# Kernel optimization log

Measured on AMD Instinct MI355X. Metric: run time of the kernel, lower is better.

## Reference

```python
import jax, jax.numpy as jnp
import numpy as np

B, S, E, H, NQ, FF = 4, 1024, 256, 32, 8, 1024
DK = E // H  # 8, equals n_wires of the quantum attention layer
EPS = 1e-5


def layernorm(x, g, b):
    mu = jnp.mean(x, axis=-1, keepdims=True)
    var = jnp.mean(jnp.square(x - mu), axis=-1, keepdims=True)
    return (x - mu) * jax.lax.rsqrt(var + EPS) * g + b


def setup_inputs() -> dict:
    key = jax.random.key(0)
    ks = jax.random.split(key, 20)
    s = lambda n: 1.0 / np.sqrt(n)
    return {
        "x": jax.random.normal(ks[0], (B, S, E), dtype=jnp.float32),
        # quantum attention trainable RX angles (one per wire)
        "theta_attn": jax.random.uniform(ks[1], (DK,), minval=-np.pi, maxval=np.pi),
        # nn.MultiheadAttention packed in-proj and out-proj
        "w_in": jax.random.normal(ks[2], (3 * E, E)) * s(E),
        "b_in": jnp.zeros((3 * E,), jnp.float32),
        "w_out": jax.random.normal(ks[3], (E, E)) * s(E),
        "b_out": jnp.zeros((E,), jnp.float32),
        # combine linear
        "w_comb": jax.random.normal(ks[4], (E, E)) * s(E),
        "b_comb": jnp.zeros((E,), jnp.float32),
        # layernorms
        "g1": jnp.ones((E,), jnp.float32), "be1": jnp.zeros((E,), jnp.float32),
        "g2": jnp.ones((E,), jnp.float32), "be2": jnp.zeros((E,), jnp.float32),
        # FFN: input_proj, quantum RY angles, linear1, linear2
        "w_ip": jax.random.normal(ks[5], (NQ, E)) * s(E),
        "b_ip": jnp.zeros((NQ,), jnp.float32),
        "theta_ffn": jax.random.uniform(ks[6], (NQ,), minval=-np.pi, maxval=np.pi),
        "w1": jax.random.normal(ks[7], (FF, NQ)) * s(NQ),
        "b1": jnp.zeros((FF,), jnp.float32),
        "w2": jax.random.normal(ks[8], (E, FF)) * s(FF),
        "b2": jnp.zeros((E,), jnp.float32),
    }


def reference(x, theta_attn, w_in, b_in, w_out, b_out, w_comb, b_comb,
              g1, be1, g2, be2, w_ip, b_ip, theta_ffn, w1, b1, w2, b2):
    batch, seq, embed = x.shape
    # ---- QuantumAttention ----
    # per-head RX(x_i) encoding followed by trainable RX(theta_i): <Z_i> = cos(x_i + theta_i)
    xh = x.reshape(batch, seq, H, DK)            # [B,S,H,dk]
    q_out = jnp.cos(xh + theta_attn).reshape(batch, seq, embed)
    # standard multi-head self-attention on q_out (q=k=v)
    qkv = q_out @ w_in.T + b_in                  # [B,S,3E]
    q, k, v = jnp.split(qkv, 3, axis=-1)
    def heads(t):
        return t.reshape(batch, seq, H, DK).transpose(0, 2, 1, 3)  # [B,H,S,dk]
    q, k, v = heads(q), heads(k), heads(v)
    scores = jnp.einsum('bhqd,bhkd->bhqk', q, k) / np.sqrt(DK)
    attn = jax.nn.softmax(scores, axis=-1)
    ctx = jnp.einsum('bhqk,bhkd->bhqd', attn, v)
    ctx = ctx.transpose(0, 2, 1, 3).reshape(batch, seq, embed)
    attn_out = (ctx @ w_out.T + b_out) @ w_comb.T + b_comb
    # ---- residual + norm1 ----
    h = layernorm(x + attn_out, g1, be1)
    # ---- QuantumFeedForward ----
    proj = h @ w_ip.T + b_ip                     # [B,S,NQ]
    # RX(x) encoding then trainable RY(phi): <Z> = cos(phi) * cos(x)
    qf = jnp.cos(theta_ffn) * jnp.cos(proj)
    ffn_out = jax.nn.relu(qf @ w1.T + b1) @ w2.T + b2
    # ---- residual + norm2 ----
    return layernorm(h + ffn_out, g2, be2)
```

## Files before the change

kernel.cpp:

```cpp
#include <hip/hip_runtime.h>
#include <hip/hip_bf16.h>

#define B_  4
#define S_  1024
#define E_  256
#define H_  32
#define DK_ 8
#define NQ_ 8
#define FF_ 1024
#define M_  (B_*S_)
#define QS  0.5100880289202462f

typedef __attribute__((ext_vector_type(8))) short bf16x8;
typedef __attribute__((ext_vector_type(4))) short short4v;
typedef __attribute__((ext_vector_type(4))) float f32x4;

__device__ inline short f2bf(float f) {
    union { float f; unsigned u; } v; v.f = f;
    unsigned r = (v.u + 0x7fff + ((v.u >> 16) & 1)) >> 16;
    return (short)r;
}

__device__ inline unsigned pk2(float a, float b) {
    __hip_bfloat162 h = __float22bfloat162_rn(make_float2(a, b));
    union { __hip_bfloat162 h; unsigned u; } c; c.h = h;
    return c.u;
}

__global__ __launch_bounds__(256) void prep_kernel(
        const float* __restrict__ x, const float* __restrict__ theta_attn,
        const float* __restrict__ w_in, const float* __restrict__ b_in,
        const float* __restrict__ w_out, const float* __restrict__ w_comb,
        const float* __restrict__ b_out, const float* __restrict__ b_comb,
        const float* __restrict__ w2,
        ushort* __restrict__ qout_bf, ushort* __restrict__ w_in_bf,
        float* __restrict__ b_in_s, ushort* __restrict__ w2_bf,
        ushort* __restrict__ w_comb_bf, ushort* __restrict__ w_outT_bf,
        float* __restrict__ zeros256, float* __restrict__ beff) {
    int blk = blockIdx.x, tid = threadIdx.x;
    __shared__ float red[4];
    if (blk < 512) {
        int i = blk * 256 + tid;
        float4 a = ((const float4*)x)[i * 2];
        float4 b = ((const float4*)x)[i * 2 + 1];
        bf16x8 o;
        o[0] = f2bf(__cosf(a.x + theta_attn[0]));
        o[1] = f2bf(__cosf(a.y + theta_attn[1]));
        o[2] = f2bf(__cosf(a.z + theta_attn[2]));
        o[3] = f2bf(__cosf(a.w + theta_attn[3]));
        o[4] = f2bf(__cosf(b.x + theta_attn[4]));
        o[5] = f2bf(__cosf(b.y + theta_attn[5]));
        o[6] = f2bf(__cosf(b.z + theta_attn[6]));
        o[7] = f2bf(__cosf(b.w + theta_attn[7]));
        *(bf16x8*)(qout_bf + (size_t)i * 8) = o;
    } else if (blk < 704) {
        int i = (blk - 512) * 256 + tid;
        float sc = (i < 16384) ? QS : 1.f;
        float4 v = ((const float4*)w_in)[i];
        short4v o = {f2bf(v.x * sc), f2bf(v.y * sc), f2bf(v.z * sc), f2bf(v.w * sc)};
        ((short4v*)w_in_bf)[i] = o;
    } else if (blk < 960) {
        int i = (blk - 704) * 256 + tid;
        float4 v = ((const float4*)w2)[i];
        short4v o = {f2bf(v.x), f2bf(v.y), f2bf(v.z), f2bf(v.w)};
        ((short4v*)w2_bf)[i] = o;
    } else if (blk < 1024) {
        int i = (blk - 960) * 256 + tid;
        float4 v = ((const float4*)w_comb)[i];
        short4v o = {f2bf(v.x), f2bf(v.y), f2bf(v.z), f2bf(v.w)};
        ((short4v*)w_comb_bf)[i] = o;
    } else if (blk < 1088) {
        int idx = (blk - 1024) * 256 + tid;
        int e = idx * 4, j = e >> 8, k0 = e & 255;
        short4v o;
#pragma unroll
        for (int i2 = 0; i2 < 4; ++i2) o[i2] = f2bf(w_out[(size_t)(k0 + i2) * 256 + j]);
        *(short4v*)(w_outT_bf + j * 256 + k0) = o;
    } else if (blk < 1089) {
        for (int r = 0; r < 3; ++r) {
            int i = r * 256 + tid;
            b_in_s[i] = b_in[i] * ((i < 256) ? QS : 1.f);
        }
        zeros256[tid] = 0.f;
    } else {
        int i = blk - 1089;
        float p = w_comb[(size_t)i * 256 + tid] * b_out[tid];
#pragma unroll
        for (int o = 32; o > 0; o >>= 1) p += __shfl_xor(p, o);
        if ((tid & 63) == 0) red[tid >> 6] = p;
        __syncthreads();
        if (tid == 0) beff[i] = red[0] + red[1] + red[2] + red[3] + b_comb[i];
    }
}

template<int OUT_BF16>
__global__ __launch_bounds__(256) void gemm_mfma_kernel(const ushort* __restrict__ A,
                                                        const ushort* __restrict__ W,
                                                        const float* __restrict__ bias,
                                                        void* __restrict__ Cv,
                                                        int Ndim, int Kdim) {
    __shared__ ushort As[128 * 64];
    __shared__ ushort Bs[64 * 64];
    int bm = blockIdx.y * 128, bn = blockIdx.x * 64;
    int tid = threadIdx.x;
    int w = tid >> 6, l = tid & 63, lq = l & 15, hi = l >> 4;
    int wm = w & 1, wn = w >> 1;
    f32x4 acc[4][2] = {};
    int srow = tid >> 3;
    int skb = (tid & 7) * 16;

    for (int k0 = 0; k0 < Kdim; k0 += 64) {
        __syncthreads();
#pragma unroll
        for (int it = 0; it < 4; ++it) {
            int row = it * 32 + srow;
            bf16x8 v = *(const bf16x8*)(A + (size_t)(bm + row) * Kdim + k0 + (skb >> 1));
            *(bf16x8*)((char*)As + row * 128 + (skb ^ ((row & 7) << 4))) = v;
        }
#pragma unroll
        for (int it = 0; it < 2; ++it) {
            int row = it * 32 + srow;
            bf16x8 v = *(const bf16x8*)(W + (size_t)(bn + row) * Kdim + k0 + (skb >> 1));
            *(bf16x8*)((char*)Bs + row * 128 + (skb ^ ((row & 7) << 4))) = v;
        }
        __syncthreads();
#pragma unroll
        for (int kk = 0; kk < 2; ++kk) {
            bf16x8 af[4], bfr[2];
#pragma unroll
            for (int mf = 0; mf < 4; ++mf) {
                int row = wm * 64 + mf * 16 + lq;
                af[mf] = *(const bf16x8*)((const char*)As + row * 128 +
                                          ((kk * 64 + hi * 16) ^ ((row & 7) << 4)));
            }
#pragma unroll
            for (int nf = 0; nf < 2; ++nf) {
                int row = wn * 32 + nf * 16 + lq;
                bfr[nf] = *(const bf16x8*)((const char*)Bs + row * 128 +
                                           ((kk * 64 + hi * 16) ^ ((row & 7) << 4)));
            }
#pragma unroll
            for (int mf = 0; mf < 4; ++mf)
#pragma unroll
                for (int nf = 0; nf < 2; ++nf)
                    acc[mf][nf] = __builtin_amdgcn_mfma_f32_16x16x32_bf16(af[mf], bfr[nf], acc[mf][nf], 0, 0, 0);
        }
    }
#pragma unroll
    for (int mf = 0; mf < 4; ++mf)
#pragma unroll
        for (int nf = 0; nf < 2; ++nf) {
            int n = bn + wn * 32 + nf * 16 + lq;
            float bv = bias[n];
#pragma unroll
            for (int r = 0; r < 4; ++r) {
                int m = bm + wm * 64 + mf * 16 + hi * 4 + r;
                float val = acc[mf][nf][r] + bv;
                if (OUT_BF16) ((ushort*)Cv)[(size_t)m * Ndim + n] = (ushort)f2bf(val);
                else ((float*)Cv)[(size_t)m * Ndim + n] = val;
            }
        }
}

__global__ __launch_bounds__(256) void attn_mfma_kernel(const ushort* __restrict__ qkv,
                                                        ushort* __restrict__ ctx) {
    __shared__ ushort smem[26696];
    const int KOFF = 0;
    const int VTOFF = 8192;
    const int POFF = 17480;
    int qt = blockIdx.x, h = blockIdx.y, b = blockIdx.z;
    int tid = threadIdx.x;
    const ushort* base = qkv + (size_t)b * S_ * (3 * E_);

    for (int i = tid; i < S_; i += 256) {
        const ushort* rp = base + (size_t)i * (3 * E_) + h * 8;
        bf16x8 kv = *(const bf16x8*)(rp + E_);
        bf16x8 vv = *(const bf16x8*)(rp + 2 * E_);
        *(bf16x8*)&smem[KOFF + i * 8] = kv;
#pragma unroll
        for (int d = 0; d < 8; ++d) smem[VTOFF + d * 1032 + i] = vv[d];
        smem[VTOFF + 8 * 1032 + i] = 0x3F80;
    }
    __syncthreads();

    int w = tid >> 6, l = tid & 63;
    int lq = l & 15, g = l >> 4;

    bf16x8 qfrag[2];
#pragma unroll
    for (int qf = 0; qf < 2; ++qf) {
        bf16x8 qv = {};
        if (g == 0)
            qv = *(const bf16x8*)(base + (size_t)(qt * 128 + w * 32 + qf * 16 + lq) * (3 * E_) + h * 8);
        qfrag[qf] = qv;
    }

    f32x4 ctxa[2] = {{0.f,0.f,0.f,0.f},{0.f,0.f,0.f,0.f}};
    ushort* Pbase0 = &smem[POFF + (w * 2 + 0) * 1152];
    ushort* Pbase1 = &smem[POFF + (w * 2 + 1) * 1152];

    for (int kt = 0; kt < 16; ++kt) {
        bf16x8 kfrag[4];
#pragma unroll
        for (int kf = 0; kf < 4; ++kf) {
            bf16x8 kv = {};
            if (g == 0) kv = *(bf16x8*)&smem[KOFF + (kt * 64 + kf * 16 + lq) * 8];
            kfrag[kf] = kv;
        }
        f32x4 st[2][4];
#pragma unroll
        for (int qf = 0; qf < 2; ++qf)
#pragma unroll
            for (int kf = 0; kf < 4; ++kf) {
                f32x4 z = {0.f, 0.f, 0.f, 0.f};
                st[qf][kf] = __builtin_amdgcn_mfma_f32_16x16x32_bf16(kfrag[kf], qfrag[qf], z, 0, 0, 0);
            }
#pragma unroll
        for (int qf = 0; qf < 2; ++qf) {
            ushort* Pb = (qf == 0) ? Pbase0 : Pbase1;
#pragma unroll
            for (int kf = 0; kf < 4; ++kf) {
                uint2 pw;
                pw.x = pk2(exp2f(st[qf][kf][0]), exp2f(st[qf][kf][1]));
                pw.y = pk2(exp2f(st[qf][kf][2]), exp2f(st[qf][kf][3]));
                *(uint2*)&Pb[lq * 72 + kf * 16 + g * 4] = pw;
            }
        }
        asm volatile("s_waitcnt lgkmcnt(0)" ::: "memory");
#pragma unroll
        for (int half = 0; half < 2; ++half) {
            bf16x8 vt = *(bf16x8*)&smem[VTOFF + lq * 1032 + kt * 64 + half * 32 + g * 8];
#pragma unroll
            for (int qf = 0; qf < 2; ++qf) {
                ushort* Pb = (qf == 0) ? Pbase0 : Pbase1;
                bf16x8 pf = *(bf16x8*)&Pb[lq * 72 + half * 32 + g * 8];
                ctxa[qf] = __builtin_amdgcn_mfma_f32_16x16x32_bf16(vt, pf, ctxa[qf], 0, 0, 0);
            }
        }
    }

#pragma unroll
    for (int qf = 0; qf < 2; ++qf) {
        float lsum = __shfl(ctxa[qf][0], 32 + lq);
        float inv = 1.f / lsum;
        if (g < 2) {
            int token = b * S_ + qt * 128 + w * 32 + qf * 16 + lq;
            short4v o = {f2bf(ctxa[qf][0] * inv), f2bf(ctxa[qf][1] * inv),
                         f2bf(ctxa[qf][2] * inv), f2bf(ctxa[qf][3] * inv)};
            *(short4v*)(ctx + (size_t)token * E_ + h * 8 + g * 4) = o;
        }
    }
}

__global__ __launch_bounds__(256) void resid_ln_kernel(const float* __restrict__ a,
                                                       const float* __restrict__ r,
                                                       const float* __restrict__ g,
                                                       const float* __restrict__ be,
                                                       float* __restrict__ out) {
    int wave = threadIdx.x >> 6, lane = threadIdx.x & 63;
    int token = blockIdx.x * 4 + wave;
    const float4 av = ((const float4*)(a + (size_t)token * E_))[lane];
    const float4 rv = ((const float4*)(r + (size_t)token * E_))[lane];
    float v0 = av.x + rv.x, v1 = av.y + rv.y, v2 = av.z + rv.z, v3 = av.w + rv.w;
    float sum = v0 + v1 + v2 + v3;
#pragma unroll
    for (int o = 32; o > 0; o >>= 1) sum += __shfl_xor(sum, o);
    float mu = sum * (1.f / E_);
    float d0 = v0 - mu, d1 = v1 - mu, d2 = v2 - mu, d3 = v3 - mu;
    float ss = d0 * d0 + d1 * d1 + d2 * d2 + d3 * d3;
#pragma unroll
    for (int o = 32; o > 0; o >>= 1) ss += __shfl_xor(ss, o);
    float rstd = rsqrtf(ss * (1.f / E_) + 1e-5f);
    float4 gv = ((const float4*)g)[lane];
    float4 bv = ((const float4*)be)[lane];
    float4 ov = make_float4(d0 * rstd * gv.x + bv.x, d1 * rstd * gv.y + bv.y,
                            d2 * rstd * gv.z + bv.z, d3 * rstd * gv.w + bv.w);
    ((float4*)(out + (size_t)token * E_))[lane] = ov;
}

__global__ __launch_bounds__(256) void projqf_kernel(const float* __restrict__ h,
                                                     const float* __restrict__ w_ip,
                                                     const float* __restrict__ b_ip,
                                                     const float* __restrict__ theta,
                                                     float* __restrict__ qf) {
    int wave = threadIdx.x >> 6, lane = threadIdx.x & 63;
    int token = blockIdx.x * 4 + wave;
    float4 hv = ((const float4*)(h + (size_t)token * E_))[lane];
    float acc[8];
#pragma unroll
    for (int w = 0; w < 8; ++w) {
        float4 wv = ((const float4*)(w_ip + w * E_))[lane];
        acc[w] = hv.x * wv.x + hv.y * wv.y + hv.z * wv.z + hv.w * wv.w;
    }
#pragma unroll
    for (int o = 32; o > 0; o >>= 1) {
#pragma unroll
        for (int w = 0; w < 8; ++w) acc[w] += __shfl_xor(acc[w], o);
    }
    if (lane == 0) {
#pragma unroll
        for (int w = 0; w < 8; ++w)
            qf[(size_t)token * NQ_ + w] = __cosf(theta[w]) * __cosf(acc[w] + b_ip[w]);
    }
}

__global__ __launch_bounds__(256) void ffn_t_kernel(const float* __restrict__ qf,
                                                    const float* __restrict__ w1,
                                                    const float* __restrict__ b1,
                                                    ushort* __restrict__ t) {
    int idx = blockIdx.x * 256 + threadIdx.x;
    int token = idx >> 7;
    int fb = (idx & 127) * 8;
    const float* qp = qf + (size_t)token * NQ_;
    float4 q0 = ((const float4*)qp)[0], q1 = ((const float4*)qp)[1];
    bf16x8 o;
#pragma unroll
    for (int j = 0; j < 8; ++j) {
        const float* wp = w1 + (size_t)(fb + j) * NQ_;
        float4 w0 = ((const float4*)wp)[0], w1v = ((const float4*)wp)[1];
        float s = b1[fb + j] + q0.x * w0.x + q0.y * w0.y + q0.z * w0.z + q0.w * w0.w
                + q1.x * w1v.x + q1.y * w1v.y + q1.z * w1v.z + q1.w * w1v.w;
        o[j] = f2bf(fmaxf(s, 0.f));
    }
    *(bf16x8*)(t + (size_t)idx * 8) = o;
}

extern "C" void kernel_launch(void* const* d_in, const int* in_sizes, int n_in,
                              void* d_out, int out_size, void* d_ws, size_t ws_size,
                              hipStream_t stream) {
    const float* x          = (const float*)d_in[0];
    const float* theta_attn = (const float*)d_in[1];
    const float* w_in       = (const float*)d_in[2];
    const float* b_in       = (const float*)d_in[3];
    const float* w_out      = (const float*)d_in[4];
    const float* b_out      = (const float*)d_in[5];
    const float* w_comb     = (const float*)d_in[6];
    const float* b_comb     = (const float*)d_in[7];
    const float* g1         = (const float*)d_in[8];
    const float* be1        = (const float*)d_in[9];
    const float* g2         = (const float*)d_in[10];
    const float* be2        = (const float*)d_in[11];
    const float* w_ip       = (const float*)d_in[12];
    const float* b_ip       = (const float*)d_in[13];
    const float* theta_ffn  = (const float*)d_in[14];
    const float* w1         = (const float*)d_in[15];
    const float* b1         = (const float*)d_in[16];
    const float* w2         = (const float*)d_in[17];
    const float* b2         = (const float*)d_in[18];
    float* out = (float*)d_out;

    char* wsb = (char*)d_ws;
    ushort* qout_bf  = (ushort*)(wsb + 0);
    ushort* qkv_bf   = (ushort*)(wsb + (2u << 20));
    ushort* t_bf     = (ushort*)(wsb + 0);
    ushort* ctx_bf   = (ushort*)(wsb + (8u << 20));
    ushort* w_comb_bf= (ushort*)(wsb + (8u << 20));
    ushort* w_outT_bf= (ushort*)(wsb + (8u << 20) + 131072);
    float*  attn_out = (float*)(wsb + (10u << 20));
    float*  ffn_out  = attn_out;
    float*  h        = (float*)(wsb + (14u << 20));
    ushort* w_in_bf  = (ushort*)(wsb + (18u << 20));
    ushort* w2_bf    = (ushort*)(wsb + (18u << 20) + 393216);
    ushort* weff_bf  = (ushort*)(wsb + (18u << 20) + 917504);
    float*  beff     = (float*)(wsb + (18u << 20) + 1048576);
    float*  zeros256 = (float*)(wsb + (18u << 20) + 1052672);
    float*  b_in_s   = (float*)(wsb + (18u << 20) + 1056768);
    float*  qf       = (float*)(wsb + (18u << 20) + 1060864);

    prep_kernel<<<1345, 256, 0, stream>>>(x, theta_attn, w_in, b_in, w_out, w_comb,
                                          b_out, b_comb, w2,
                                          qout_bf, w_in_bf, b_in_s, w2_bf,
                                          w_comb_bf, w_outT_bf, zeros256, beff);
    gemm_mfma_kernel<1><<<dim3(4, 2), 256, 0, stream>>>(w_comb_bf, w_outT_bf, zeros256, weff_bf, E_, E_);
    gemm_mfma_kernel<1><<<dim3(768 / 64, M_ / 128), 256, 0, stream>>>(qout_bf, w_in_bf, b_in_s, qkv_bf, 768, E_);
    attn_mfma_kernel<<<dim3(S_ / 128, H_, B_), 256, 0, stream>>>(qkv_bf, ctx_bf);
    gemm_mfma_kernel<0><<<dim3(E_ / 64, M_ / 128), 256, 0, stream>>>(ctx_bf, weff_bf, beff, attn_out, E_, E_);
    resid_ln_kernel<<<M_ / 4, 256, 0, stream>>>(x, attn_out, g1, be1, h);
    projqf_kernel<<<M_ / 4, 256, 0, stream>>>(h, w_ip, b_ip, theta_ffn, qf);
    ffn_t_kernel<<<(M_ * FF_) / (256 * 8), 256, 0, stream>>>(qf, w1, b1, t_bf);
    gemm_mfma_kernel<0><<<dim3(E_ / 64, M_ / 128), 256, 0, stream>>>(t_bf, w2_bf, b2, ffn_out, E_, FF_);
    resid_ln_kernel<<<M_ / 4, 256, 0, stream>>>(h, ffn_out, g2, be2, out);
}
```

Baseline: 209.0 us.

## Keep attention probabilities in registers and fuse LayerNorm1 with FFN input projection

The attention kernel stops writing the exponentiated scores to shared memory. It swaps the MFMA operand order so the P tile stays in registers as the A operand. To match, the transposed V tile is stored in a permuted column order with a padded stride, and K is read straight from global memory instead of being staged in LDS. This cuts LDS traffic and sync waits and raises occupancy via launch bounds, at the cost of scattered per-element output stores. Separately, the first residual LayerNorm and the FFN input projection are merged into one kernel, removing one launch and a re-read of h.

```diff
diff --git a/kernel.cpp b/kernel.cpp
--- a/kernel.cpp
+++ b/kernel.cpp
@@ -10,6 +10,7 @@
 #define FF_ 1024
 #define M_  (B_*S_)
 #define QS  0.5100880289202462f
+#define VSTRIDE 1036
 
 typedef __attribute__((ext_vector_type(8))) short bf16x8;
 typedef __attribute__((ext_vector_type(4))) short short4v;
@@ -162,93 +163,130 @@
         }
 }
 
-__global__ __launch_bounds__(256) void attn_mfma_kernel(const ushort* __restrict__ qkv,
-                                                        ushort* __restrict__ ctx) {
-    __shared__ ushort smem[26696];
-    const int KOFF = 0;
-    const int VTOFF = 8192;
-    const int POFF = 17480;
+__global__ __launch_bounds__(256, 4) void attn_mfma_kernel(const ushort* __restrict__ qkv,
+                                                           ushort* __restrict__ ctx) {
+    __shared__ ushort vt[9 * VSTRIDE + 4];
     int qt = blockIdx.x, h = blockIdx.y, b = blockIdx.z;
     int tid = threadIdx.x;
-    const ushort* base = qkv + (size_t)b * S_ * (3 * E_);
+    const ushort* base = qkv + (size_t)b * S_ * (3 * E_) + h * 8;
 
     for (int i = tid; i < S_; i += 256) {
-        const ushort* rp = base + (size_t)i * (3 * E_) + h * 8;
-        bf16x8 kv = *(const bf16x8*)(rp + E_);
-        bf16x8 vv = *(const bf16x8*)(rp + 2 * E_);
-        *(bf16x8*)&smem[KOFF + i * 8] = kv;
-#pragma unroll
-        for (int d = 0; d < 8; ++d) smem[VTOFF + d * 1032 + i] = vv[d];
-        smem[VTOFF + 8 * 1032 + i] = 0x3F80;
+        bf16x8 vv = *(const bf16x8*)(base + (size_t)i * (3 * E_) + 2 * E_);
+        int kf = (i >> 4) & 3, hh = (i >> 2) & 3, s = i & 3;
+        int pv = (i & ~63) + ((kf >> 1) << 5) + (hh << 3) + ((kf & 1) << 2) + s;
+#pragma unroll
+        for (int d = 0; d < 8; ++d) vt[d * VSTRIDE + pv] = vv[d];
+        vt[8 * VSTRIDE + pv] = 0x3F80;
     }
     __syncthreads();
 
-    int w = tid >> 6, l = tid & 63;
-    int lq = l & 15, g = l >> 4;
+    int w = tid >> 6, l = tid & 63, lq = l & 15, g = l >> 4;
 
     bf16x8 qfrag[2];
 #pragma unroll
     for (int qf = 0; qf < 2; ++qf) {
         bf16x8 qv = {};
         if (g == 0)
-            qv = *(const bf16x8*)(base + (size_t)(qt * 128 + w * 32 + qf * 16 + lq) * (3 * E_) + h * 8);
+            qv = *(const bf16x8*)(base + (size_t)(qt * 128 + w * 32 + qf * 16 + lq) * (3 * E_));
         qfrag[qf] = qv;
     }
 
     f32x4 ctxa[2] = {{0.f,0.f,0.f,0.f},{0.f,0.f,0.f,0.f}};
-    ushort* Pbase0 = &smem[POFF + (w * 2 + 0) * 1152];
-    ushort* Pbase1 = &smem[POFF + (w * 2 + 1) * 1152];
 
     for (int kt = 0; kt < 16; ++kt) {
         bf16x8 kfrag[4];
 #pragma unroll
         for (int kf = 0; kf < 4; ++kf) {
             bf16x8 kv = {};
-            if (g == 0) kv = *(bf16x8*)&smem[KOFF + (kt * 64 + kf * 16 + lq) * 8];
+            if (g == 0)
+                kv = *(const bf16x8*)(base + (size_t)(kt * 64 + kf * 16 + lq) * (3 * E_) + E_);
             kfrag[kf] = kv;
         }
-        f32x4 st[2][4];
-#pragma unroll
-        for (int qf = 0; qf < 2; ++qf)
+        bf16x8 vf0 = *(bf16x8*)&vt[lq * VSTRIDE + kt * 64 + g * 8];
+        bf16x8 vf1 = *(bf16x8*)&vt[lq * VSTRIDE + kt * 64 + 32 + g * 8];
+#pragma unroll
+        for (int qf = 0; qf < 2; ++qf) {
+            f32x4 st[4];
 #pragma unroll
             for (int kf = 0; kf < 4; ++kf) {
                 f32x4 z = {0.f, 0.f, 0.f, 0.f};
-                st[qf][kf] = __builtin_amdgcn_mfma_f32_16x16x32_bf16(kfrag[kf], qfrag[qf], z, 0, 0, 0);
+                st[kf] = __builtin_amdgcn_mfma_f32_16x16x32_bf16(kfrag[kf], qfrag[qf], z, 0, 0, 0);
             }
-#pragma unroll
-        for (int qf = 0; qf < 2; ++qf) {
-            ushort* Pb = (qf == 0) ? Pbase0 : Pbase1;
-#pragma unroll
-            for (int kf = 0; kf < 4; ++kf) {
-                uint2 pw;
-                pw.x = pk2(exp2f(st[qf][kf][0]), exp2f(st[qf][kf][1]));
-                pw.y = pk2(exp2f(st[qf][kf][2]), exp2f(st[qf][kf][3]));
-                *(uint2*)&Pb[lq * 72 + kf * 16 + g * 4] = pw;
-            }
-        }
-        asm volatile("s_waitcnt lgkmcnt(0)" ::: "memory");
-#pragma unroll
-        for (int half = 0; half < 2; ++half) {
-            bf16x8 vt = *(bf16x8*)&smem[VTOFF + lq * 1032 + kt * 64 + half * 32 + g * 8];
-#pragma unroll
-            for (int qf = 0; qf < 2; ++qf) {
-                ushort* Pb = (qf == 0) ? Pbase0 : Pbase1;
-                bf16x8 pf = *(bf16x8*)&Pb[lq * 72 + half * 32 + g * 8];
-                ctxa[qf] = __builtin_amdgcn_mfma_f32_16x16x32_bf16(vt, pf, ctxa[qf], 0, 0, 0);
-            }
+            union { unsigned u[4]; bf16x8 v; } p0, p1;
+            p0.u[0] = pk2(exp2f(st[0][0]), exp2f(st[0][1]));
+            p0.u[1] = pk2(exp2f(st[0][2]), exp2f(st[0][3]));
+            p0.u[2] = pk2(exp2f(st[1][0]), exp2f(st[1][1]));
+            p0.u[3] = pk2(exp2f(st[1][2]), exp2f(st[1][3]));
+            p1.u[0] = pk2(exp2f(st[2][0]), exp2f(st[2][1]));
+            p1.u[1] = pk2(exp2f(st[2][2]), exp2f(st[2][3]));
+            p1.u[2] = pk2(exp2f(st[3][0]), exp2f(st[3][1]));
+            p1.u[3] = pk2(exp2f(st[3][2]), exp2f(st[3][3]));
+            ctxa[qf] = __builtin_amdgcn_mfma_f32_16x16x32_bf16(p0.v, vf0, ctxa[qf], 0, 0, 0);
+            ctxa[qf] = __builtin_amdgcn_mfma_f32_16x16x32_bf16(p1.v, vf1, ctxa[qf], 0, 0, 0);
         }
     }
 
 #pragma unroll
     for (int qf = 0; qf < 2; ++qf) {
-        float lsum = __shfl(ctxa[qf][0], 32 + lq);
-        float inv = 1.f / lsum;
-        if (g < 2) {
-            int token = b * S_ + qt * 128 + w * 32 + qf * 16 + lq;
-            short4v o = {f2bf(ctxa[qf][0] * inv), f2bf(ctxa[qf][1] * inv),
-                         f2bf(ctxa[qf][2] * inv), f2bf(ctxa[qf][3] * inv)};
-            *(short4v*)(ctx + (size_t)token * E_ + h * 8 + g * 4) = o;
-        }
+        int src = (l & 48) + 8;
+        float s0 = __shfl(ctxa[qf][0], src);
+        float s1 = __shfl(ctxa[qf][1], src);
+        float s2 = __shfl(ctxa[qf][2], src);
+        float s3 = __shfl(ctxa[qf][3], src);
+        if (lq < 8) {
+            int tok = b * S_ + qt * 128 + w * 32 + qf * 16 + g * 4;
+            ushort* cp = ctx + (size_t)tok * E_ + h * 8 + lq;
+            cp[0]       = (ushort)f2bf(ctxa[qf][0] / s0);
+            cp[E_]      = (ushort)f2bf(ctxa[qf][1] / s1);
+            cp[2 * E_]  = (ushort)f2bf(ctxa[qf][2] / s2);
+            cp[3 * E_]  = (ushort)f2bf(ctxa[qf][3] / s3);
+        }
+    }
+}
+
+__global__ __launch_bounds__(256) void ln1_projqf_kernel(const float* __restrict__ a,
+                                                         const float* __restrict__ r,
+                                                         const float* __restrict__ g,
+                                                         const float* __restrict__ be,
+                                                         const float* __restrict__ w_ip,
+                                                         const float* __restrict__ b_ip,
+                                                         const float* __restrict__ theta,
+                                                         float* __restrict__ h,
+                                                         float* __restrict__ qf) {
+    int wave = threadIdx.x >> 6, lane = threadIdx.x & 63;
+    int token = blockIdx.x * 4 + wave;
+    const float4 av = ((const float4*)(a + (size_t)token * E_))[lane];
+    const float4 rv = ((const float4*)(r + (size_t)token * E_))[lane];
+    float v0 = av.x + rv.x, v1 = av.y + rv.y, v2 = av.z + rv.z, v3 = av.w + rv.w;
+    float sum = v0 + v1 + v2 + v3;
+#pragma unroll
+    for (int o = 32; o > 0; o >>= 1) sum += __shfl_xor(sum, o);
+    float mu = sum * (1.f / E_);
+    float d0 = v0 - mu, d1 = v1 - mu, d2 = v2 - mu, d3 = v3 - mu;
+    float ss = d0 * d0 + d1 * d1 + d2 * d2 + d3 * d3;
+#pragma unroll
+    for (int o = 32; o > 0; o >>= 1) ss += __shfl_xor(ss, o);
+    float rstd = rsqrtf(ss * (1.f / E_) + 1e-5f);
+    float4 gv = ((const float4*)g)[lane];
+    float4 bv = ((const float4*)be)[lane];
+    float4 hv = make_float4(d0 * rstd * gv.x + bv.x, d1 * rstd * gv.y + bv.y,
+                            d2 * rstd * gv.z + bv.z, d3 * rstd * gv.w + bv.w);
+    ((float4*)(h + (size_t)token * E_))[lane] = hv;
+    float acc[8];
+#pragma unroll
+    for (int w = 0; w < 8; ++w) {
+        float4 wv = ((const float4*)(w_ip + w * E_))[lane];
+        acc[w] = hv.x * wv.x + hv.y * wv.y + hv.z * wv.z + hv.w * wv.w;
+    }
+#pragma unroll
+    for (int o = 32; o > 0; o >>= 1) {
+#pragma unroll
+        for (int w = 0; w < 8; ++w) acc[w] += __shfl_xor(acc[w], o);
+    }
+    if (lane == 0) {
+#pragma unroll
+        for (int w = 0; w < 8; ++w)
+            qf[(size_t)token * NQ_ + w] = __cosf(theta[w]) * __cosf(acc[w] + b_ip[w]);
     }
 }
 
@@ -276,32 +314,6 @@
     float4 ov = make_float4(d0 * rstd * gv.x + bv.x, d1 * rstd * gv.y + bv.y,
                             d2 * rstd * gv.z + bv.z, d3 * rstd * gv.w + bv.w);
     ((float4*)(out + (size_t)token * E_))[lane] = ov;
-}
-
-__global__ __launch_bounds__(256) void projqf_kernel(const float* __restrict__ h,
-                                                     const float* __restrict__ w_ip,
-                                                     const float* __restrict__ b_ip,
-                                                     const float* __restrict__ theta,
-                                                     float* __restrict__ qf) {
-    int wave = threadIdx.x >> 6, lane = threadIdx.x & 63;
-    int token = blockIdx.x * 4 + wave;
-    float4 hv = ((const float4*)(h + (size_t)token * E_))[lane];
-    float acc[8];
-#pragma unroll
-    for (int w = 0; w < 8; ++w) {
-        float4 wv = ((const float4*)(w_ip + w * E_))[lane];
-        acc[w] = hv.x * wv.x + hv.y * wv.y + hv.z * wv.z + hv.w * wv.w;
-    }
-#pragma unroll
-    for (int o = 32; o > 0; o >>= 1) {
-#pragma unroll
-        for (int w = 0; w < 8; ++w) acc[w] += __shfl_xor(acc[w], o);
-    }
-    if (lane == 0) {
-#pragma unroll
-        for (int w = 0; w < 8; ++w)
-            qf[(size_t)token * NQ_ + w] = __cosf(theta[w]) * __cosf(acc[w] + b_ip[w]);
-    }
 }
 
 __global__ __launch_bounds__(256) void ffn_t_kernel(const float* __restrict__ qf,
@@ -375,8 +387,7 @@
     gemm_mfma_kernel<1><<<dim3(768 / 64, M_ / 128), 256, 0, stream>>>(qout_bf, w_in_bf, b_in_s, qkv_bf, 768, E_);
     attn_mfma_kernel<<<dim3(S_ / 128, H_, B_), 256, 0, stream>>>(qkv_bf, ctx_bf);
     gemm_mfma_kernel<0><<<dim3(E_ / 64, M_ / 128), 256, 0, stream>>>(ctx_bf, weff_bf, beff, attn_out, E_, E_);
-    resid_ln_kernel<<<M_ / 4, 256, 0, stream>>>(x, attn_out, g1, be1, h);
-    projqf_kernel<<<M_ / 4, 256, 0, stream>>>(h, w_ip, b_ip, theta_ffn, qf);
+    ln1_projqf_kernel<<<M_ / 4, 256, 0, stream>>>(x, attn_out, g1, be1, w_ip, b_ip, theta_ffn, h, qf);
     ffn_t_kernel<<<(M_ * FF_) / (256 * 8), 256, 0, stream>>>(qf, w1, b1, t_bf);
     gemm_mfma_kernel<0><<<dim3(E_ / 64, M_ / 128), 256, 0, stream>>>(t_bf, w2_bf, b2, ffn_out, E_, FF_);
     resid_ln_kernel<<<M_ / 4, 256, 0, stream>>>(h, ffn_out, g2, be2, out);
```

Measured after the change: 204.9 us. About the same (-1.9%).
